# Kernel optimization log

Hardware: AMD Instinct MI355X
Metric: run time of the kernel (lower is better)

The kernel has to match this reference:

```python
import jax, jax.numpy as jnp
import numpy as np

RHO = 1.0          # ADMM penalty
LAM = 0.1          # lambda_sparse
MAX_ITERS = 20
ZETA = 0.05        # APAS drift threshold / CDS temperature
TAU = 0.1          # chiral stabilizer tolerance
STEP = 0.1         # gradient step size
COHESION = 1.0     # Mohr-Coulomb cohesion
MU = 0.5           # Mohr-Coulomb friction coefficient
DP_K = 10.0        # Drucker-Prager deviatoric-norm radius


def _pas(c):
    # Phase Alignment Invariant: scalar phase-coherence metric in [0,1]
    return jnp.abs(jnp.mean(jnp.cos(c)))


def _chirality(c):
    # odd (sign-sensitive) global moment
    return jnp.mean(c ** 3)


def _mc_proj(c, g):
    # Mohr-Coulomb yield projection: clamp magnitude to cohesion + mu*|grad|
    return jnp.sign(c) * jnp.minimum(jnp.abs(c), COHESION + MU * jnp.abs(g))


def _dp_proj(c):
    # Drucker-Prager: project deviatoric part onto norm ball of radius DP_K (per row)
    m = jnp.mean(c, axis=-1, keepdims=True)
    dev = c - m
    n = jnp.linalg.norm(dev, axis=-1, keepdims=True)
    scale = jnp.minimum(1.0, DP_K / (n + 1e-8))
    return m + dev * scale


def setup_inputs() -> dict:
    key = jax.random.key(0)
    k1, k2, k3 = jax.random.split(key, 3)
    B, D = 1024, 2048
    initial_c = 0.5 * jax.random.normal(k1, (B, D), dtype=jnp.float32)
    W = jax.random.normal(k2, (D, D), dtype=jnp.float32) / np.float32(np.sqrt(D))
    love_w = 1.0 + 0.01 * jax.random.normal(k3, (D,), dtype=jnp.float32)
    love_b = jnp.zeros((D,), dtype=jnp.float32)
    return {"initial_c": initial_c, "W": W, "love_w": love_w, "love_b": love_b}


def _forward(initial_c, W, love_w, love_b):
    c_sym = initial_c
    c0 = initial_c
    z0 = c0
    u0 = jnp.zeros_like(c0)
    prev_pas0 = _pas(c0)
    prev_score0 = -_chirality(c0)  # drift = 0 -> exp(0) = 1

    def step(carry, _):
        c, z, u, prev_pas, prev_score, low, done = carry

        def energy(ci):
            pred = ci @ W  # forward_op_fn
            violation_pressure = 0.5 * jnp.sum((pred - ci) ** 2)
            admm_tension = 0.5 * RHO * jnp.sum((ci - z + u) ** 2)
            return violation_pressure + admm_tension

        g = jax.grad(energy)(c)
        c_yield = _mc_proj(c, g)
        c_next = (c_yield * love_w + love_b) - STEP * g  # LoveVector then step
        z_in = c_next + u
        thr = LAM / RHO
        z_next = jnp.sign(z_in) * jnp.maximum(jnp.abs(z_in) - thr, 0.0)
        u_next = u + (c_next - z_next)

        cur_pas = _pas(c_next)
        drift = jnp.abs(cur_pas - prev_pas)
        violation = drift > ZETA
        low = jnp.where(cur_pas < 0.5, low + 1, 0)
        done = done | (low > 20)
        cur_score = -_chirality(c_next) * jnp.exp(-drift / ZETA)
        stable = (cur_score - prev_score) >= -TAU
        acc = (~violation) & stable & (~done)

        sel = lambda a, b: jnp.where(acc, a, b)
        new = (sel(c_next, c), sel(z_next, z), sel(u_next, u),
               jnp.where(acc, cur_pas, prev_pas),
               jnp.where(acc, cur_score, prev_score), low, done)
        return new, None

    init = (c0, z0, u0, prev_pas0, prev_score0,
            jnp.zeros((), jnp.int32), jnp.zeros((), jnp.bool_))
    (c_phys, z, u, _, _, _, _), _ = jax.lax.scan(step, init, None, length=MAX_ITERS)

    diff = jnp.linalg.norm(c_phys - c_sym)
    chi_cur = _chirality(c_phys)
    chi_orig = _chirality(c_sym)
    status = jnp.where(jnp.sign(chi_cur) != jnp.sign(chi_orig),
                       2,
                       jnp.where(diff > 5.0, 2, jnp.where(diff > 1.0, 1, 0))).astype(jnp.int32)

    delta = c_phys - c_sym
    symbolic_delta = jnp.round(delta * 10.0) / 10.0
    c_compressed = _dp_proj(c_sym + symbolic_delta)
    return c_compressed, status


def reference(initial_c, W, love_w, love_b):
    return _forward(initial_c, W, love_w, love_b)
```

## Files before the change

### kernel.cpp

```cpp
#include <hip/hip_runtime.h>
#include <math.h>

#define D 2048
#define BROWS 1024
#define NEL (D*BROWS)
#define NBLK 1024
#define NTHREADS_TOT (NBLK*256)

#define GM 64
#define GN 128
#define GK 32

__device__ __forceinline__ double blk_reduce(double v, double* sm) {
    const int t = threadIdx.x;
    sm[t] = v;
    __syncthreads();
    for (int s = 128; s > 0; s >>= 1) {
        if (t < s) sm[t] += sm[t + s];
        __syncthreads();
    }
    double r = sm[0];
    __syncthreads();
    return r;
}

__global__ __launch_bounds__(256) void k_gemm(const float* __restrict__ A,
        const float* __restrict__ B, float* __restrict__ P0, float* __restrict__ P1,
        const float* __restrict__ Wadj, int ksz, int mode, const int* __restrict__ frz,
        int nx, int ypg)
{
    if (frz && *frz) return;
    __shared__ float As[GK][GM + 4];
    __shared__ float Bs[GK][GN + 4];
    const int t  = threadIdx.x;
    const int tx = t & 15, ty = t >> 4;

    const int wg  = blockIdx.x;
    const int xcd = wg & 7;
    const int idx = wg >> 3;
    const int y   = xcd + 8 * (idx % ypg);
    const int tmp = idx / ypg;
    const int x   = tmp % nx;
    const int zz  = tmp / nx;

    const int row0 = y * GM, col0 = x * GN;
    const int k0 = zz * ksz;
    float* __restrict__ out = zz ? P1 : P0;

    float acc[4][8];
    #pragma unroll
    for (int i = 0; i < 4; ++i)
        #pragma unroll
        for (int j = 0; j < 8; ++j) acc[i][j] = 0.0f;

    for (int kt = 0; kt < ksz; kt += GK) {
        const int kb = k0 + kt;
        #pragma unroll
        for (int v = 0; v < 2; ++v) {
            const int vid = t + v * 256;
            const int r = vid >> 3, q = vid & 7;
            const float4 ga = *reinterpret_cast<const float4*>(
                &A[(size_t)(row0 + r) * D + kb + q * 4]);
            As[q*4+0][r] = ga.x; As[q*4+1][r] = ga.y;
            As[q*4+2][r] = ga.z; As[q*4+3][r] = ga.w;
        }
        #pragma unroll
        for (int v = 0; v < 4; ++v) {
            const int vid = t + v * 256;
            const int r = vid >> 3, q = vid & 7;
            const float4 gb = *reinterpret_cast<const float4*>(
                &B[(size_t)(col0 + r) * D + kb + q * 4]);
            Bs[q*4+0][r] = gb.x; Bs[q*4+1][r] = gb.y;
            Bs[q*4+2][r] = gb.z; Bs[q*4+3][r] = gb.w;
        }
        __syncthreads();
        #pragma unroll
        for (int k = 0; k < GK; ++k) {
            float a[4], b[8];
            *reinterpret_cast<float4*>(&a[0]) = *reinterpret_cast<const float4*>(&As[k][ty*4]);
            *reinterpret_cast<float4*>(&b[0]) = *reinterpret_cast<const float4*>(&Bs[k][tx*4]);
            *reinterpret_cast<float4*>(&b[4]) = *reinterpret_cast<const float4*>(&Bs[k][64 + tx*4]);
            #pragma unroll
            for (int i = 0; i < 4; ++i)
                #pragma unroll
                for (int j = 0; j < 8; ++j)
                    acc[i][j] += a[i] * b[j];
        }
        __syncthreads();
    }

    #pragma unroll
    for (int i = 0; i < 4; ++i) {
        const int grow = row0 + ty*4 + i;
        float vv[8];
        #pragma unroll
        for (int j = 0; j < 8; ++j) vv[j] = acc[i][j];
        if (mode == 0) {
            #pragma unroll
            for (int j = 0; j < 8; ++j) {
                const int gcol = col0 + ((j < 4) ? (tx*4 + j) : (64 + tx*4 + j - 4));
                const float wsum = Wadj[(size_t)grow * D + gcol] + Wadj[(size_t)gcol * D + grow];
                vv[j] += (grow == gcol ? 1.0f : 0.0f) - wsum;
            }
        }
        float* orow = &out[(size_t)grow * D + col0];
        *reinterpret_cast<float4*>(&orow[tx*4]) =
            make_float4(vv[0], vv[1], vv[2], vv[3]);
        *reinterpret_cast<float4*>(&orow[64 + tx*4]) =
            make_float4(vv[4], vv[5], vv[6], vv[7]);
    }
}

__global__ __launch_bounds__(256) void k_init(const float* __restrict__ c0,
        float* __restrict__ c, float* __restrict__ z, float* __restrict__ u,
        double* __restrict__ partials)
{
    __shared__ double sm[256];
    double sc = 0.0, s3 = 0.0;
    const int tid = blockIdx.x * 256 + threadIdx.x;
    const float4 zero4 = make_float4(0.f, 0.f, 0.f, 0.f);
    for (int i4 = tid; i4 < NEL/4; i4 += NTHREADS_TOT) {
        const float4 v4 = reinterpret_cast<const float4*>(c0)[i4];
        reinterpret_cast<float4*>(c)[i4] = v4;
        reinterpret_cast<float4*>(z)[i4] = v4;
        reinterpret_cast<float4*>(u)[i4] = zero4;
        const float va[4] = {v4.x, v4.y, v4.z, v4.w};
        #pragma unroll
        for (int L = 0; L < 4; ++L) {
            sc += (double)cosf(va[L]);
            s3 += (double)((va[L] * va[L]) * va[L]);
        }
    }
    const double tc = blk_reduce(sc, sm);
    const double t3 = blk_reduce(s3, sm);
    if (threadIdx.x == 0) { partials[blockIdx.x] = tc; partials[NBLK + blockIdx.x] = t3; }
}

__global__ __launch_bounds__(256) void k_decide0(const double* __restrict__ partials,
        double* __restrict__ scal, int* __restrict__ flag, int* __restrict__ frz,
        int* __restrict__ sel)
{
    __shared__ double sm[256];
    const int t = threadIdx.x;
    const double a = partials[t] + partials[t+256] + partials[t+512] + partials[t+768];
    const double b = partials[NBLK+t] + partials[NBLK+t+256] + partials[NBLK+t+512] + partials[NBLK+t+768];
    const double tc = blk_reduce(a, sm);
    const double t3 = blk_reduce(b, sm);
    if (t == 0) {
        const double pas = fabs(tc / (double)NEL);
        const double chi = t3 / (double)NEL;
        scal[0] = pas; scal[1] = -chi; scal[2] = chi;
        *flag = 0; *frz = 0; *sel = 0;
    }
}

__global__ __launch_bounds__(256) void k_elem_pp(const float* __restrict__ P0,
        const float* __restrict__ P1, const float* __restrict__ cc,
        float* __restrict__ cn, float* __restrict__ z, float* __restrict__ u,
        const float* __restrict__ lw, const float* __restrict__ lb,
        double* __restrict__ partials, const int* __restrict__ frz)
{
#pragma clang fp contract(off)
    if (*frz) return;
    __shared__ double sm[256];
    double sc = 0.0, s3 = 0.0;
    const int tid = blockIdx.x * 256 + threadIdx.x;
    for (int i4 = tid; i4 < NEL/4; i4 += NTHREADS_TOT) {
        const int j4 = i4 & (D/4 - 1);
        const float4 p0 = reinterpret_cast<const float4*>(P0)[i4];
        const float4 p1 = reinterpret_cast<const float4*>(P1)[i4];
        const float4 cv4 = reinterpret_cast<const float4*>(cc)[i4];
        const float4 zv4 = reinterpret_cast<const float4*>(z)[i4];
        const float4 uv4 = reinterpret_cast<const float4*>(u)[i4];
        const float4 w4 = reinterpret_cast<const float4*>(lw)[j4];
        const float4 b4 = reinterpret_cast<const float4*>(lb)[j4];
        const float p0a[4] = {p0.x, p0.y, p0.z, p0.w};
        const float p1a[4] = {p1.x, p1.y, p1.z, p1.w};
        const float cva[4] = {cv4.x, cv4.y, cv4.z, cv4.w};
        const float zva[4] = {zv4.x, zv4.y, zv4.z, zv4.w};
        const float uva[4] = {uv4.x, uv4.y, uv4.z, uv4.w};
        const float w4a[4] = {w4.x, w4.y, w4.z, w4.w};
        const float b4a[4] = {b4.x, b4.y, b4.z, b4.w};
        float Rc[4], Rz[4], Ru[4];
        #pragma unroll
        for (int L = 0; L < 4; ++L) {
            const float cv = cva[L];
            const float uv = uva[L];
            const float g = (p0a[L] + p1a[L]) + ((cv - zva[L]) + uv);
            const float lim = 1.0f + 0.5f * fabsf(g);
            const float mn = fminf(fabsf(cv), lim);
            const float cy = (cv > 0.0f) ? mn : ((cv < 0.0f) ? -mn : 0.0f);
            const float cnv = (cy * w4a[L] + b4a[L]) - 0.1f * g;
            Rc[L] = cnv;
            const float zi = cnv + uv;
            float zm = fabsf(zi) - 0.1f;
            zm = fmaxf(zm, 0.0f);
            const float zn = (zi > 0.0f) ? zm : ((zi < 0.0f) ? -zm : 0.0f);
            Rz[L] = zn;
            Ru[L] = uv + (cnv - zn);
            sc += (double)cosf(cnv);
            s3 += (double)((cnv * cnv) * cnv);
        }
        reinterpret_cast<float4*>(cn)[i4] = make_float4(Rc[0], Rc[1], Rc[2], Rc[3]);
        reinterpret_cast<float4*>(z)[i4]  = make_float4(Rz[0], Rz[1], Rz[2], Rz[3]);
        reinterpret_cast<float4*>(u)[i4]  = make_float4(Ru[0], Ru[1], Ru[2], Ru[3]);
    }
    const double tc = blk_reduce(sc, sm);
    const double t3 = blk_reduce(s3, sm);
    if (threadIdx.x == 0) { partials[blockIdx.x] = tc; partials[NBLK + blockIdx.x] = t3; }
}

__global__ __launch_bounds__(256) void k_elem(float* __restrict__ P0,
        const float* __restrict__ P1, const float* __restrict__ c,
        const float* __restrict__ z, const float* __restrict__ u,
        const float* __restrict__ lw, const float* __restrict__ lb,
        double* __restrict__ partials, const int* __restrict__ frz)
{
#pragma clang fp contract(off)
    if (*frz) return;
    __shared__ double sm[256];
    double sc = 0.0, s3 = 0.0;
    const int tid = blockIdx.x * 256 + threadIdx.x;
    for (int i = tid; i < NEL; i += NTHREADS_TOT) {
        const int j = i & (D - 1);
        const float cv = c[i];
        const float g = (P0[i] + P1[i]) + ((cv - z[i]) + u[i]);
        const float lim = 1.0f + 0.5f * fabsf(g);
        const float mn = fminf(fabsf(cv), lim);
        const float cy = (cv > 0.0f) ? mn : ((cv < 0.0f) ? -mn : 0.0f);
        const float cnv = (cy * lw[j] + lb[j]) - 0.1f * g;
        P0[i] = cnv;
        sc += (double)cosf(cnv);
        s3 += (double)((cnv * cnv) * cnv);
    }
    const double tc = blk_reduce(sc, sm);
    const double t3 = blk_reduce(s3, sm);
    if (threadIdx.x == 0) { partials[blockIdx.x] = tc; partials[NBLK + blockIdx.x] = t3; }
}

__global__ __launch_bounds__(256) void k_decide(const double* __restrict__ partials,
        double* __restrict__ scal, int* __restrict__ flag, int* __restrict__ frz,
        int* __restrict__ sel, int next_sel)
{
    __shared__ double sm[256];
    if (*frz) return;
    const int t = threadIdx.x;
    const double a = partials[t] + partials[t+256] + partials[t+512] + partials[t+768];
    const double b = partials[NBLK+t] + partials[NBLK+t+256] + partials[NBLK+t+512] + partials[NBLK+t+768];
    const double tc = blk_reduce(a, sm);
    const double t3 = blk_reduce(b, sm);
    if (t == 0) {
        const double pas = fabs(tc / (double)NEL);
        const double drift = fabs(pas - scal[0]);
        const double chi = t3 / (double)NEL;
        const double score = -chi * exp(-drift / 0.05);
        const bool violation = drift > 0.05;
        const bool stable = (score - scal[1]) >= -0.1;
        const int acc = (!violation && stable) ? 1 : 0;
        *flag = acc;
        if (acc) { scal[0] = pas; scal[1] = score; *sel = next_sel; }
        else     { *frz = 1; }
    }
}

__global__ __launch_bounds__(256) void k_commit(const float* __restrict__ cn,
        float* __restrict__ c, float* __restrict__ z, float* __restrict__ u,
        const int* __restrict__ flag)
{
#pragma clang fp contract(off)
    if (*flag == 0) return;
    const int tid = blockIdx.x * 256 + threadIdx.x;
    for (int i = tid; i < NEL; i += NTHREADS_TOT) {
        const float cnv = cn[i];
        const float uv = u[i];
        const float zi = cnv + uv;
        float zm = fabsf(zi) - 0.1f;
        zm = fmaxf(zm, 0.0f);
        const float zn = (zi > 0.0f) ? zm : ((zi < 0.0f) ? -zm : 0.0f);
        c[i] = cnv;
        z[i] = zn;
        u[i] = uv + (cnv - zn);
    }
}

__global__ __launch_bounds__(256) void k_final_rows(const float* __restrict__ c0,
        const float* __restrict__ cA, const float* __restrict__ cB,
        const int* __restrict__ sel, float* __restrict__ outp)
{
#pragma clang fp contract(off)
    __shared__ double sm[256];
    const float* __restrict__ c = (*sel) ? cB : cA;
    const int row = blockIdx.x;
    const size_t base = (size_t)row * D;
    float tv[8];
    double s1 = 0.0;
    #pragma unroll
    for (int s = 0; s < 8; ++s) {
        const int j = threadIdx.x + s * 256;
        const float s0 = c0[base + j];
        const float delta = c[base + j] - s0;
        const float sym = rintf(delta * 10.0f) / 10.0f;
        const float tval = s0 + sym;
        tv[s] = tval;
        s1 += (double)tval;
    }
    const double tot = blk_reduce(s1, sm);
    const float m = (float)(tot / (double)D);
    double s2 = 0.0;
    #pragma unroll
    for (int s = 0; s < 8; ++s) {
        const float dev = tv[s] - m;
        s2 += (double)(dev * dev);
    }
    const double tot2 = blk_reduce(s2, sm);
    const float n = sqrtf((float)tot2);
    const float scale = fminf(1.0f, 10.0f / (n + 1e-8f));
    #pragma unroll
    for (int s = 0; s < 8; ++s) {
        const int j = threadIdx.x + s * 256;
        outp[base + j] = m + (tv[s] - m) * scale;
    }
}

__global__ __launch_bounds__(256) void k_final_glob(const float* __restrict__ c0,
        const float* __restrict__ cA, const float* __restrict__ cB,
        const int* __restrict__ sel, double* __restrict__ partials)
{
    __shared__ double sm[256];
    const float* __restrict__ c = (*sel) ? cB : cA;
    double s3 = 0.0, sd = 0.0;
    const int tid = blockIdx.x * 256 + threadIdx.x;
    for (int i = tid; i < NEL; i += NTHREADS_TOT) {
        const float v = c[i];
        s3 += (double)((v * v) * v);
        const float d = v - c0[i];
        sd += (double)(d * d);
    }
    const double t3 = blk_reduce(s3, sm);
    const double td = blk_reduce(sd, sm);
    if (threadIdx.x == 0) { partials[blockIdx.x] = t3; partials[NBLK + blockIdx.x] = td; }
}

__global__ __launch_bounds__(256) void k_final_status(const double* __restrict__ partials,
        const double* __restrict__ scal, float* __restrict__ outp)
{
    __shared__ double sm[256];
    const int t = threadIdx.x;
    const double a = partials[t] + partials[t+256] + partials[t+512] + partials[t+768];
    const double b = partials[NBLK+t] + partials[NBLK+t+256] + partials[NBLK+t+512] + partials[NBLK+t+768];
    const double t3 = blk_reduce(a, sm);
    const double td = blk_reduce(b, sm);
    if (t == 0) {
        const double chi_cur = t3 / (double)NEL;
        const double diff = sqrt(td);
        const double chi_orig = scal[2];
        const int s_cur = (chi_cur > 0.0) - (chi_cur < 0.0);
        const int s_org = (chi_orig > 0.0) - (chi_orig < 0.0);
        int status;
        if (s_cur != s_org)   status = 2;
        else if (diff > 5.0)  status = 2;
        else if (diff > 1.0)  status = 1;
        else                  status = 0;
        outp[NEL] = (float)status;
    }
}

extern "C" void kernel_launch(void* const* d_in, const int* in_sizes, int n_in,
                              void* d_out, int out_size, void* d_ws, size_t ws_size,
                              hipStream_t stream)
{
    const float* c0 = (const float*)d_in[0];
    const float* W  = (const float*)d_in[1];
    const float* lw = (const float*)d_in[2];
    const float* lb = (const float*)d_in[3];
    float* outp = (float*)d_out;

    const size_t M4 = (size_t)D * D;
    const size_t N4 = (size_t)NEL;
    float* Mb = (float*)d_ws;
    float* region = Mb + M4;

    const size_t tail_bytes = (2 * NBLK + 8) * sizeof(double) + 4 * sizeof(int);
    const bool pp = ws_size >= (M4 + 6 * N4) * sizeof(float) + tail_bytes;

    float *cA, *cB, *z, *u, *P0, *P1;
    if (pp) { cA = region; cB = cA + N4; z = cB + N4; u = z + N4; P0 = u + N4; P1 = P0 + N4; }
    else    { cA = region; cB = cA;      z = cA + N4; u = z + N4; P0 = u + N4; P1 = P0 + N4; }
    double* partials = (double*)(P1 + N4);
    double* scal = partials + 2 * NBLK;
    int* flag = (int*)(scal + 8);
    int* frz  = flag + 1;
    int* sel  = frz + 1;

    k_gemm<<<512, 256, 0, stream>>>(W, W, Mb, Mb, W, D, 0, nullptr, 16, 4);
    k_init<<<NBLK, 256, 0, stream>>>(c0, cA, z, u, partials);
    k_decide0<<<1, 256, 0, stream>>>(partials, scal, flag, frz, sel);

    for (int t = 0; t < 20; ++t) {
        const float* ccur = (pp && (t & 1)) ? cB : cA;
        float* cnxt = (pp && !(t & 1)) ? cB : cA;
        k_gemm<<<512, 256, 0, stream>>>(ccur, Mb, P0, P1, nullptr, D / 2, 1, frz, 16, 2);
        if (pp) {
            k_elem_pp<<<NBLK, 256, 0, stream>>>(P0, P1, ccur, cnxt, z, u, lw, lb, partials, frz);
            k_decide<<<1, 256, 0, stream>>>(partials, scal, flag, frz, sel, (t + 1) & 1);
        } else {
            k_elem<<<NBLK, 256, 0, stream>>>(P0, P1, cA, z, u, lw, lb, partials, frz);
            k_decide<<<1, 256, 0, stream>>>(partials, scal, flag, frz, sel, 0);
            k_commit<<<NBLK, 256, 0, stream>>>(P0, cA, z, u, flag);
        }
    }

    k_final_rows<<<BROWS, 256, 0, stream>>>(c0, cA, cB, sel, outp);
    k_final_glob<<<NBLK, 256, 0, stream>>>(c0, cA, cB, sel, partials);
    k_final_status<<<1, 256, 0, stream>>>(partials, scal, outp);
}
```

Before: 3.071 ms.

## Register-prefetch GEMM tiles and fuse decide kernels via last-block reduction

The GEMM now loads the next K-slice into registers while the current shared tile is computed, with a smaller K tile, a 2-blocks-per-CU launch bound, and a plain 3D grid replacing the XCD-swizzled block mapping. The separate single-block decide/status kernels are merged into the preceding reduction kernels using an atomic counter, where the last block performs the final reduction. This removes about 20 tiny launches and overlaps global loads with FMA work. The trade-off is extra atomics and fences, and possibly worse L2 locality without the XCD swizzle.

```diff
diff --git a/kernel.cpp b/kernel.cpp
--- a/kernel.cpp
+++ b/kernel.cpp
@@ -9,7 +9,7 @@
 
 #define GM 64
 #define GN 128
-#define GK 32
+#define GK 16
 
 __device__ __forceinline__ double blk_reduce(double v, double* sm) {
     const int t = threadIdx.x;
@@ -24,28 +24,23 @@
     return r;
 }
 
-__global__ __launch_bounds__(256) void k_gemm(const float* __restrict__ A,
+__global__ __launch_bounds__(256, 2) void k_gemm(const float* __restrict__ A,
         const float* __restrict__ B, float* __restrict__ P0, float* __restrict__ P1,
-        const float* __restrict__ Wadj, int ksz, int mode, const int* __restrict__ frz,
-        int nx, int ypg)
+        const float* __restrict__ Wadj, int ksz, int mode, const int* __restrict__ frz)
 {
     if (frz && *frz) return;
     __shared__ float As[GK][GM + 4];
     __shared__ float Bs[GK][GN + 4];
     const int t  = threadIdx.x;
     const int tx = t & 15, ty = t >> 4;
-
-    const int wg  = blockIdx.x;
-    const int xcd = wg & 7;
-    const int idx = wg >> 3;
-    const int y   = xcd + 8 * (idx % ypg);
-    const int tmp = idx / ypg;
-    const int x   = tmp % nx;
-    const int zz  = tmp / nx;
-
-    const int row0 = y * GM, col0 = x * GN;
-    const int k0 = zz * ksz;
-    float* __restrict__ out = zz ? P1 : P0;
+    const int row0 = blockIdx.y * GM, col0 = blockIdx.x * GN;
+    const int k0 = blockIdx.z * ksz;
+    float* __restrict__ out = blockIdx.z ? P1 : P0;
+
+    const int wr = t >> 2, wq = t & 3;
+    const float* pA  = A + (size_t)(row0 + wr) * D + (k0 + wq * 4);
+    const float* pB0 = B + (size_t)(col0 + wr) * D + (k0 + wq * 4);
+    const float* pB1 = B + (size_t)(col0 + 64 + wr) * D + (k0 + wq * 4);
 
     float acc[4][8];
     #pragma unroll
@@ -53,27 +48,26 @@
         #pragma unroll
         for (int j = 0; j < 8; ++j) acc[i][j] = 0.0f;
 
-    for (int kt = 0; kt < ksz; kt += GK) {
-        const int kb = k0 + kt;
-        #pragma unroll
-        for (int v = 0; v < 2; ++v) {
-            const int vid = t + v * 256;
-            const int r = vid >> 3, q = vid & 7;
-            const float4 ga = *reinterpret_cast<const float4*>(
-                &A[(size_t)(row0 + r) * D + kb + q * 4]);
-            As[q*4+0][r] = ga.x; As[q*4+1][r] = ga.y;
-            As[q*4+2][r] = ga.z; As[q*4+3][r] = ga.w;
-        }
-        #pragma unroll
-        for (int v = 0; v < 4; ++v) {
-            const int vid = t + v * 256;
-            const int r = vid >> 3, q = vid & 7;
-            const float4 gb = *reinterpret_cast<const float4*>(
-                &B[(size_t)(col0 + r) * D + kb + q * 4]);
-            Bs[q*4+0][r] = gb.x; Bs[q*4+1][r] = gb.y;
-            Bs[q*4+2][r] = gb.z; Bs[q*4+3][r] = gb.w;
-        }
+    const int ntiles = ksz / GK;
+    float4 ga  = *reinterpret_cast<const float4*>(pA);
+    float4 gb0 = *reinterpret_cast<const float4*>(pB0);
+    float4 gb1 = *reinterpret_cast<const float4*>(pB1);
+    pA += GK; pB0 += GK; pB1 += GK;
+
+    for (int tt = 0; tt < ntiles; ++tt) {
+        As[wq*4+0][wr] = ga.x;  As[wq*4+1][wr] = ga.y;
+        As[wq*4+2][wr] = ga.z;  As[wq*4+3][wr] = ga.w;
+        Bs[wq*4+0][wr] = gb0.x; Bs[wq*4+1][wr] = gb0.y;
+        Bs[wq*4+2][wr] = gb0.z; Bs[wq*4+3][wr] = gb0.w;
+        Bs[wq*4+0][wr+64] = gb1.x; Bs[wq*4+1][wr+64] = gb1.y;
+        Bs[wq*4+2][wr+64] = gb1.z; Bs[wq*4+3][wr+64] = gb1.w;
         __syncthreads();
+        if (tt + 1 < ntiles) {
+            ga  = *reinterpret_cast<const float4*>(pA);
+            gb0 = *reinterpret_cast<const float4*>(pB0);
+            gb1 = *reinterpret_cast<const float4*>(pB1);
+            pA += GK; pB0 += GK; pB1 += GK;
+        }
         #pragma unroll
         for (int k = 0; k < GK; ++k) {
             float a[4], b[8];
@@ -113,9 +107,11 @@
 
 __global__ __launch_bounds__(256) void k_init(const float* __restrict__ c0,
         float* __restrict__ c, float* __restrict__ z, float* __restrict__ u,
-        double* __restrict__ partials)
-{
-    __shared__ double sm[256];
+        double* __restrict__ partials, double* __restrict__ scal,
+        int* __restrict__ counter)
+{
+    __shared__ double sm[256];
+    __shared__ int islast;
     double sc = 0.0, s3 = 0.0;
     const int tid = blockIdx.x * 256 + threadIdx.x;
     const float4 zero4 = make_float4(0.f, 0.f, 0.f, 0.f);
@@ -133,24 +129,24 @@
     }
     const double tc = blk_reduce(sc, sm);
     const double t3 = blk_reduce(s3, sm);
-    if (threadIdx.x == 0) { partials[blockIdx.x] = tc; partials[NBLK + blockIdx.x] = t3; }
-}
-
-__global__ __launch_bounds__(256) void k_decide0(const double* __restrict__ partials,
-        double* __restrict__ scal, int* __restrict__ flag, int* __restrict__ frz,
-        int* __restrict__ sel)
-{
-    __shared__ double sm[256];
+    if (threadIdx.x == 0) {
+        partials[blockIdx.x] = tc; partials[NBLK + blockIdx.x] = t3;
+        __threadfence();
+        islast = (atomicAdd(counter, 1) == NBLK - 1);
+    }
+    __syncthreads();
+    if (!islast) return;
+    __threadfence();
     const int t = threadIdx.x;
     const double a = partials[t] + partials[t+256] + partials[t+512] + partials[t+768];
     const double b = partials[NBLK+t] + partials[NBLK+t+256] + partials[NBLK+t+512] + partials[NBLK+t+768];
-    const double tc = blk_reduce(a, sm);
-    const double t3 = blk_reduce(b, sm);
+    const double tc2 = blk_reduce(a, sm);
+    const double t32 = blk_reduce(b, sm);
     if (t == 0) {
-        const double pas = fabs(tc / (double)NEL);
-        const double chi = t3 / (double)NEL;
+        *counter = 0;
+        const double pas = fabs(tc2 / (double)NEL);
+        const double chi = t32 / (double)NEL;
         scal[0] = pas; scal[1] = -chi; scal[2] = chi;
-        *flag = 0; *frz = 0; *sel = 0;
     }
 }
 
@@ -158,11 +154,14 @@
         const float* __restrict__ P1, const float* __restrict__ cc,
         float* __restrict__ cn, float* __restrict__ z, float* __restrict__ u,
         const float* __restrict__ lw, const float* __restrict__ lb,
-        double* __restrict__ partials, const int* __restrict__ frz)
+        double* __restrict__ partials, int* __restrict__ frz,
+        double* __restrict__ scal, int* __restrict__ sel,
+        int* __restrict__ counter, int next_sel)
 {
 #pragma clang fp contract(off)
     if (*frz) return;
     __shared__ double sm[256];
+    __shared__ int islast;
     double sc = 0.0, s3 = 0.0;
     const int tid = blockIdx.x * 256 + threadIdx.x;
     for (int i4 = tid; i4 < NEL/4; i4 += NTHREADS_TOT) {
@@ -207,7 +206,30 @@
     }
     const double tc = blk_reduce(sc, sm);
     const double t3 = blk_reduce(s3, sm);
-    if (threadIdx.x == 0) { partials[blockIdx.x] = tc; partials[NBLK + blockIdx.x] = t3; }
+    if (threadIdx.x == 0) {
+        partials[blockIdx.x] = tc; partials[NBLK + blockIdx.x] = t3;
+        __threadfence();
+        islast = (atomicAdd(counter, 1) == NBLK - 1);
+    }
+    __syncthreads();
+    if (!islast) return;
+    __threadfence();
+    const int t = threadIdx.x;
+    const double a = partials[t] + partials[t+256] + partials[t+512] + partials[t+768];
+    const double b = partials[NBLK+t] + partials[NBLK+t+256] + partials[NBLK+t+512] + partials[NBLK+t+768];
+    const double tc2 = blk_reduce(a, sm);
+    const double t32 = blk_reduce(b, sm);
+    if (t == 0) {
+        *counter = 0;
+        const double pas = fabs(tc2 / (double)NEL);
+        const double drift = fabs(pas - scal[0]);
+        const double chi = t32 / (double)NEL;
+        const double score = -chi * exp(-drift / 0.05);
+        const bool violation = drift > 0.05;
+        const bool stable = (score - scal[1]) >= -0.1;
+        if (!violation && stable) { scal[0] = pas; scal[1] = score; *sel = next_sel; }
+        else                      { *frz = 1; }
+    }
 }
 
 __global__ __launch_bounds__(256) void k_elem(float* __restrict__ P0,
@@ -324,9 +346,12 @@
 
 __global__ __launch_bounds__(256) void k_final_glob(const float* __restrict__ c0,
         const float* __restrict__ cA, const float* __restrict__ cB,
-        const int* __restrict__ sel, double* __restrict__ partials)
-{
-    __shared__ double sm[256];
+        const int* __restrict__ sel, double* __restrict__ partials,
+        const double* __restrict__ scal, float* __restrict__ outp,
+        int* __restrict__ counter)
+{
+    __shared__ double sm[256];
+    __shared__ int islast;
     const float* __restrict__ c = (*sel) ? cB : cA;
     double s3 = 0.0, sd = 0.0;
     const int tid = blockIdx.x * 256 + threadIdx.x;
@@ -338,21 +363,23 @@
     }
     const double t3 = blk_reduce(s3, sm);
     const double td = blk_reduce(sd, sm);
-    if (threadIdx.x == 0) { partials[blockIdx.x] = t3; partials[NBLK + blockIdx.x] = td; }
-}
-
-__global__ __launch_bounds__(256) void k_final_status(const double* __restrict__ partials,
-        const double* __restrict__ scal, float* __restrict__ outp)
-{
-    __shared__ double sm[256];
+    if (threadIdx.x == 0) {
+        partials[blockIdx.x] = t3; partials[NBLK + blockIdx.x] = td;
+        __threadfence();
+        islast = (atomicAdd(counter, 1) == NBLK - 1);
+    }
+    __syncthreads();
+    if (!islast) return;
+    __threadfence();
     const int t = threadIdx.x;
     const double a = partials[t] + partials[t+256] + partials[t+512] + partials[t+768];
     const double b = partials[NBLK+t] + partials[NBLK+t+256] + partials[NBLK+t+512] + partials[NBLK+t+768];
-    const double t3 = blk_reduce(a, sm);
-    const double td = blk_reduce(b, sm);
+    const double t32 = blk_reduce(a, sm);
+    const double td2 = blk_reduce(b, sm);
     if (t == 0) {
-        const double chi_cur = t3 / (double)NEL;
-        const double diff = sqrt(td);
+        *counter = 0;
+        const double chi_cur = t32 / (double)NEL;
+        const double diff = sqrt(td2);
         const double chi_orig = scal[2];
         const int s_cur = (chi_cur > 0.0) - (chi_cur < 0.0);
         const int s_org = (chi_orig > 0.0) - (chi_orig < 0.0);
@@ -380,7 +407,7 @@
     float* Mb = (float*)d_ws;
     float* region = Mb + M4;
 
-    const size_t tail_bytes = (2 * NBLK + 8) * sizeof(double) + 4 * sizeof(int);
+    const size_t tail_bytes = (2 * NBLK + 8) * sizeof(double) + 8 * sizeof(int);
     const bool pp = ws_size >= (M4 + 6 * N4) * sizeof(float) + tail_bytes;
 
     float *cA, *cB, *z, *u, *P0, *P1;
@@ -391,18 +418,20 @@
     int* flag = (int*)(scal + 8);
     int* frz  = flag + 1;
     int* sel  = frz + 1;
-
-    k_gemm<<<512, 256, 0, stream>>>(W, W, Mb, Mb, W, D, 0, nullptr, 16, 4);
-    k_init<<<NBLK, 256, 0, stream>>>(c0, cA, z, u, partials);
-    k_decide0<<<1, 256, 0, stream>>>(partials, scal, flag, frz, sel);
+    int* counter = sel + 1;
+
+    hipMemsetAsync(flag, 0, 4 * sizeof(int), stream);
+
+    k_gemm<<<dim3(D / GN, D / GM, 1), 256, 0, stream>>>(W, W, Mb, Mb, W, D, 0, nullptr);
+    k_init<<<NBLK, 256, 0, stream>>>(c0, cA, z, u, partials, scal, counter);
 
     for (int t = 0; t < 20; ++t) {
         const float* ccur = (pp && (t & 1)) ? cB : cA;
         float* cnxt = (pp && !(t & 1)) ? cB : cA;
-        k_gemm<<<512, 256, 0, stream>>>(ccur, Mb, P0, P1, nullptr, D / 2, 1, frz, 16, 2);
+        k_gemm<<<dim3(D / GN, BROWS / GM, 2), 256, 0, stream>>>(ccur, Mb, P0, P1, nullptr, D / 2, 1, frz);
         if (pp) {
-            k_elem_pp<<<NBLK, 256, 0, stream>>>(P0, P1, ccur, cnxt, z, u, lw, lb, partials, frz);
-            k_decide<<<1, 256, 0, stream>>>(partials, scal, flag, frz, sel, (t + 1) & 1);
+            k_elem_pp<<<NBLK, 256, 0, stream>>>(P0, P1, ccur, cnxt, z, u, lw, lb,
+                                                partials, frz, scal, sel, counter, (t + 1) & 1);
         } else {
             k_elem<<<NBLK, 256, 0, stream>>>(P0, P1, cA, z, u, lw, lb, partials, frz);
             k_decide<<<1, 256, 0, stream>>>(partials, scal, flag, frz, sel, 0);
@@ -411,6 +440,5 @@
     }
 
     k_final_rows<<<BROWS, 256, 0, stream>>>(c0, cA, cB, sel, outp);
-    k_final_glob<<<NBLK, 256, 0, stream>>>(c0, cA, cB, sel, partials);
-    k_final_status<<<1, 256, 0, stream>>>(partials, scal, outp);
-}
+    k_final_glob<<<NBLK, 256, 0, stream>>>(c0, cA, cB, sel, partials, scal, outp, counter);
+}
```

After: 3.589 ms. +16.9%, slower.
